# Optimization experiments

Measured on AMD Instinct MI355X. Metric: run time of the kernel, lower is better.

## Reference

```python
import jax, jax.numpy as jnp
import numpy as np
from jax import lax

DG = 16          # deformable_groups
K = 9            # 3x3 kernel taps
PAD = 1
MAX_RES = 10.0   # max_residue_magnitude


def conv3x3(x, w, b):
    # NCHW / OIHW, stride 1, SAME padding (pad=1 for 3x3)
    return lax.conv_general_dilated(x, w, (1, 1), 'SAME',
                                    dimension_numbers=('NCHW', 'OIHW', 'NCHW')) + b[None, :, None, None]


def lrelu(x):
    return jnp.where(x >= 0, x, 0.1 * x)


def setup_inputs() -> dict:
    key = jax.random.key(0)
    ks = jax.random.split(key, 10)
    B, C, H, W = 4, 64, 128, 128
    Cout = 64
    coff_in = 2 * C + 2          # (1 + pa_frames//2)*C + pa_frames, pa_frames=2
    nch = 3 * K * DG             # 432 offset/mask channels

    def mkw(k, o, i, scale=1.0):
        return jax.random.normal(k, (o, i, 3, 3), jnp.float32) * (scale / np.sqrt(i * 9))

    return {
        'x': jax.random.normal(ks[0], (B, C, H, W), jnp.float32),
        'x_flow_warped': jax.random.normal(ks[1], (B, C, H, W), jnp.float32),
        'x_current': jax.random.normal(ks[2], (B, C, H, W), jnp.float32),
        'flow': jax.random.normal(ks[3], (B, 2, H, W), jnp.float32) * 2.0,
        'w1': mkw(ks[4], Cout, coff_in), 'b1': jnp.zeros((Cout,), jnp.float32),
        'w2': mkw(ks[5], Cout, Cout),    'b2': jnp.zeros((Cout,), jnp.float32),
        'w3': mkw(ks[6], Cout, Cout),    'b3': jnp.zeros((Cout,), jnp.float32),
        'w4': mkw(ks[7], nch, Cout, 0.1), 'b4': jnp.zeros((nch,), jnp.float32),
        'weight': mkw(ks[8], Cout, C),   'bias': jnp.zeros((Cout,), jnp.float32),
    }


def deform_conv2d(x, offset, mask, weight, bias):
    # modulated deformable conv, 3x3, stride 1, pad 1, dilation 1, groups=1
    B, C, H, W = x.shape
    O = weight.shape[0]
    dg, Cg = DG, C // DG
    off = offset.reshape(B, dg, K, 2, H, W)
    dy, dx = off[:, :, :, 0], off[:, :, :, 1]        # (B,dg,K,H,W), (y,x) pairs
    ki = jnp.arange(3)
    ii, jj = jnp.meshgrid(ki, ki, indexing='ij')
    ii = ii.reshape(K).astype(jnp.float32)
    jj = jj.reshape(K).astype(jnp.float32)
    # sampling coords in input space: h - pad + i + dy, w - pad + j + dx
    py = dy + (jnp.arange(H, dtype=jnp.float32) - PAD)[None, None, None, :, None] + ii[None, None, :, None, None]
    px = dx + (jnp.arange(W, dtype=jnp.float32) - PAD)[None, None, None, None, :] + jj[None, None, :, None, None]
    y0 = jnp.floor(py)
    x0 = jnp.floor(px)
    wy1 = py - y0
    wx1 = px - x0
    y0i = y0.astype(jnp.int32)
    x0i = x0.astype(jnp.int32)
    xg = x.reshape(B, dg, Cg, H * W)

    def gather(yi, xi):
        valid = ((yi >= 0) & (yi < H) & (xi >= 0) & (xi < W)).astype(x.dtype)  # zero outside
        idx = (jnp.clip(yi, 0, H - 1) * W + jnp.clip(xi, 0, W - 1)).reshape(B, dg, 1, K * H * W)
        v = jnp.take_along_axis(xg, jnp.broadcast_to(idx, (B, dg, Cg, K * H * W)), axis=-1)
        return v.reshape(B, dg, Cg, K, H, W) * valid[:, :, None]

    s = (gather(y0i, x0i)         * ((1 - wy1) * (1 - wx1))[:, :, None]
         + gather(y0i, x0i + 1)   * ((1 - wy1) * wx1)[:, :, None]
         + gather(y0i + 1, x0i)   * (wy1 * (1 - wx1))[:, :, None]
         + gather(y0i + 1, x0i + 1) * (wy1 * wx1)[:, :, None])
    s = s * mask.reshape(B, dg, 1, K, H, W)
    s = s.reshape(B, C, K, H, W)
    return jnp.einsum('bckhw,ock->bohw', s, weight.reshape(O, C, K)) + bias[None, :, None, None]


def reference(x, x_flow_warped, x_current, flow, w1, b1, w2, b2, w3, b3, w4, b4, weight, bias):
    feat = jnp.concatenate([x_flow_warped, x_current, flow], axis=1)
    h = lrelu(conv3x3(feat, w1, b1))
    h = lrelu(conv3x3(h, w2, b2))
    h = lrelu(conv3x3(h, w3, b3))
    out = conv3x3(h, w4, b4)
    o1, o2, mask = jnp.split(out, 3, axis=1)
    offset = MAX_RES * jnp.tanh(jnp.concatenate([o1, o2], axis=1))
    flowf = flow[:, ::-1]  # flip (x,y) -> (y,x)
    offset = offset + jnp.tile(flowf, (1, offset.shape[1] // 2, 1, 1))
    mask = jax.nn.sigmoid(mask)
    return deform_conv2d(x, offset, mask, weight, bias)
```

## Files before the change

### kernel.cpp

```cpp
#include <hip/hip_runtime.h>
#include <math.h>
#include <type_traits>

#define BH 4
#define HH 128
#define WW 128
#define HW (HH * WW)
#define SSTR 600

typedef __attribute__((ext_vector_type(8))) short bf16x8;
typedef __attribute__((ext_vector_type(4))) float f32x4;

typedef const __attribute__((address_space(1))) void* as1_t;
typedef __attribute__((address_space(3))) void* as3_t;

__device__ inline short f2bf(float f) {
    union { float f; unsigned u; } x; x.f = f;
    unsigned r = x.u + 0x7fff + ((x.u >> 16) & 1);
    return (short)(r >> 16);
}
__device__ inline float bf2f(short h) {
    union { unsigned u; float f; } x; x.u = ((unsigned)(unsigned short)h) << 16;
    return x.f;
}
__device__ inline float bflo(unsigned u) {
    union { unsigned u; float f; } x; x.u = u << 16; return x.f;
}
__device__ inline float bfhi(unsigned u) {
    union { unsigned u; float f; } x; x.u = u & 0xffff0000u; return x.f;
}

struct RepackArgs {
    const float* w[5];
    short* dst[5];
    short* zero;
    int off[6];
};

__device__ inline void repack_generic(const float* w, short* dst, int g,
                                      int M, int Cin, int T, int MT)
{
    int lane = g & 63;
    int f = g >> 6;
    int mt = f % MT;
    int kt = f / MT;
    int tap = kt % T;
    int kc = kt / T;
    int m = mt * 16 + (lane & 15);
    int ic0 = kc * 32 + (lane >> 4) * 8;
    short v[8];
#pragma unroll
    for (int i = 0; i < 8; ++i) {
        int ic = ic0 + i;
        float x = (m < M && ic < Cin) ? w[((size_t)m * Cin + ic) * T + tap] : 0.f;
        v[i] = f2bf(x);
    }
    *(bf16x8*)(dst + (size_t)g * 8) = *(const bf16x8*)v;
}

__global__ __launch_bounds__(256) void repack_all_k(RepackArgs a)
{
    int g = blockIdx.x * 256 + threadIdx.x;
    if (g < a.off[1]) {
        repack_generic(a.w[0], a.dst[0], g - a.off[0], 64, 130, 9, 4);
    } else if (g < a.off[2]) {
        repack_generic(a.w[1], a.dst[1], g - a.off[1], 64, 64, 9, 4);
    } else if (g < a.off[3]) {
        repack_generic(a.w[2], a.dst[2], g - a.off[2], 64, 64, 9, 4);
    } else if (g < a.off[4]) {
        repack_generic(a.w[3], a.dst[3], g - a.off[3], 432, 64, 9, 27);
    } else if (g < a.off[5]) {
        int gg = g - a.off[4];
        int lane = gg & 63;
        int f = gg >> 6;
        int mt = f & 3, kc = f >> 2;
        int m = mt * 16 + (lane & 15);
        int ck0 = kc * 32 + (lane >> 4) * 8;
        short v[8];
#pragma unroll
        for (int i = 0; i < 8; ++i) {
            int ck = ck0 + i;
            int dg = ck / 36, rem = ck % 36;
            int k = rem >> 2, cg = rem & 3;
            int c = dg * 4 + cg;
            v[i] = f2bf(a.w[4][((size_t)m * 64 + c) * 9 + k]);
        }
        *(bf16x8*)(a.dst[4] + (size_t)gg * 8) = *(const bf16x8*)v;
    } else if (g < a.off[5] + 8) {
        uint2 z; z.x = 0; z.y = 0;
        *(uint2*)(a.zero + (size_t)(g - a.off[5]) * 4) = z;
    }
}

__global__ __launch_bounds__(256) void prep_k(
    const float* __restrict__ xfw, const float* __restrict__ xcur,
    const float* __restrict__ flow, const float* __restrict__ x,
    short* __restrict__ cc, short* __restrict__ xt)
{
    int tid = threadIdx.x;
    int z = blockIdx.z;
    int px = blockIdx.x * 256 + tid;
    if (z < BH) {
        int b = z;
        const float* s0 = xfw + (size_t)b * 64 * HW + px;
        const float* s1 = xcur + (size_t)b * 64 * HW + px;
        const float* s2 = flow + (size_t)b * 2 * HW + px;
        short v[144];
#pragma unroll
        for (int c = 0; c < 64; ++c) v[c] = f2bf(s0[(size_t)c * HW]);
#pragma unroll
        for (int c = 0; c < 64; ++c) v[64 + c] = f2bf(s1[(size_t)c * HW]);
        v[128] = f2bf(s2[0]);
        v[129] = f2bf(s2[HW]);
#pragma unroll
        for (int c = 130; c < 144; ++c) v[c] = 0;
        short* dst = cc + ((size_t)b * HW + px) * 144;
#pragma unroll
        for (int q = 0; q < 18; ++q)
            *(bf16x8*)(dst + q * 8) = *(const bf16x8*)&v[q * 8];
    } else {
        int b = z - BH;
        const float* src = x + (size_t)b * 64 * HW + px;
        short v[64];
#pragma unroll
        for (int c = 0; c < 64; ++c) v[c] = f2bf(src[(size_t)c * HW]);
        short* dstb = xt + (size_t)b * 16 * HW * 4 + (size_t)px * 4;
#pragma unroll
        for (int d = 0; d < 16; ++d)
            *(uint2*)(dstb + (size_t)d * HW * 4) = *(const uint2*)&v[d * 4];
    }
}

template<int CSTR, int KC, bool ACT, int MTW>
__global__ __launch_bounds__(256) void conv_mfma_k(
    const short* __restrict__ in, const short* __restrict__ wp,
    const float* __restrict__ bias, const short* __restrict__ zerobuf,
    short* __restrict__ out, int Cout, int MB, int MT)
{
    __shared__ alignas(16) short X[4 * 198 * 8];
    const int tid = threadIdx.x;
    const int lane = tid & 63, wv = tid >> 6;
    const int x0 = blockIdx.x * 64, y = blockIdx.y;
    const int zb = blockIdx.z;
    const int b = zb / MB, mb = zb % MB;

    int mtg[MTW];
#pragma unroll
    for (int mt = 0; mt < MTW; ++mt) {
        int t = (mb * 4 + wv) * MTW + mt;
        mtg[mt] = (t < MT) ? t : MT - 1;
    }

    const int r = tid / 66, c = tid - r * 66;
    const int yy = y + r - 1, xx = x0 + c - 1;
    const bool stg = (tid < 198);
    const bool inb = stg && (yy >= 0 && yy < HH && xx >= 0 && xx < WW);
    const short* srcp = inb ? (in + ((size_t)b * HW + (size_t)yy * WW + xx) * CSTR)
                            : zerobuf;

    f32x4 acc[MTW][4] = {};

    for (int kc = 0; kc < KC; ++kc) {
        __syncthreads();
        if (stg) {
            const short* gp = inb ? (srcp + kc * 32) : srcp;
#pragma unroll
            for (int g = 0; g < 4; ++g) {
                __builtin_amdgcn_global_load_lds(
                    (as1_t)(const void*)(gp + g * 8),
                    (as3_t)(void*)&X[((size_t)g * 198 + wv * 64) * 8],
                    16, 0, 0);
            }
        }
        __syncthreads();
#pragma unroll
        for (int tap = 0; tap < 9; ++tap) {
            const int dy = tap / 3, dx = tap - dy * 3;
            bf16x8 a[MTW];
#pragma unroll
            for (int mt = 0; mt < MTW; ++mt)
                a[mt] = *(const bf16x8*)(wp + (((size_t)(kc * 9 + tap) * MT + mtg[mt]) * 64 + lane) * 8);
#pragma unroll
            for (int nt = 0; nt < 4; ++nt) {
                int cc2 = nt * 16 + (lane & 15) + dx;
                bf16x8 bb = *(const bf16x8*)&X[(((lane >> 4) * 198) + dy * 66 + cc2) * 8];
#pragma unroll
                for (int mt = 0; mt < MTW; ++mt)
                    acc[mt][nt] = __builtin_amdgcn_mfma_f32_16x16x32_bf16(a[mt], bb, acc[mt][nt], 0, 0, 0);
            }
        }
    }

    const int xl = lane & 15, rg = lane >> 4;
#pragma unroll
    for (int mt = 0; mt < MTW; ++mt) {
        int t = (mb * 4 + wv) * MTW + mt;
        int m0 = t * 16;
        if (m0 >= Cout) continue;
#pragma unroll
        for (int nt = 0; nt < 4; ++nt) {
            int xx2 = x0 + nt * 16 + xl;
            short pk[4];
#pragma unroll
            for (int j = 0; j < 4; ++j) {
                int o = m0 + rg * 4 + j;
                float rv = acc[mt][nt][j] + bias[o];
                if (ACT) rv = (rv >= 0.f) ? rv : 0.1f * rv;
                pk[j] = f2bf(rv);
            }
            *(uint2*)(out + ((size_t)b * HW + (size_t)y * WW + xx2) * (size_t)Cout
                      + m0 + rg * 4) = *(const uint2*)pk;
        }
    }
}

__global__ __launch_bounds__(256) void dcn_k(
    const short* __restrict__ xt, const float* __restrict__ flow,
    const short* __restrict__ out4, const short* __restrict__ wtp,
    const float* __restrict__ bias, float* __restrict__ out)
{
    __shared__ alignas(16) short s[16 * SSTR];
    const int tid = threadIdx.x;
    const int b = blockIdx.z, y = blockIdx.y, xb = blockIdx.x * 16;
    const size_t hw = (size_t)HW;
    constexpr float L2E = 1.4426950408889634f;

    const int lane = tid & 63, wv = tid >> 6;
    const int p = tid & 15;
    const int dg = tid >> 4;
    const int xp = xb + p;
    const size_t pix = (size_t)y * WW + xp;
    const short* xg = xt + ((size_t)b * 16 + dg) * hw * 4;
    const short* o4p = out4 + ((size_t)b * hw + pix) * 432;
    const float fl0 = flow[((size_t)b * 2 + 0) * hw + pix];
    const float fl1 = flow[((size_t)b * 2 + 1) * hw + pix];

    const unsigned* pd = (const unsigned*)o4p + 9 * dg;
    const short* pm = o4p + 288 + 9 * dg;
    short* sp = &s[p * SSTR + dg * 36];

#pragma unroll
    for (int it = 0; it < 9; ++it) {
        unsigned dyx = pd[it];
        float omk = bf2f(pm[it]);
        float ody = bflo(dyx), odx = bfhi(dyx);
        float tdy = 1.f - 2.f * __builtin_amdgcn_rcpf(__builtin_amdgcn_exp2f(2.f * L2E * ody) + 1.f);
        float tdx = 1.f - 2.f * __builtin_amdgcn_rcpf(__builtin_amdgcn_exp2f(2.f * L2E * odx) + 1.f);
        float m   = __builtin_amdgcn_rcpf(1.f + __builtin_amdgcn_exp2f(-L2E * omk));

        float py = 10.f * tdy + fl1 + (float)(y  - 1 + it / 3);
        float px = 10.f * tdx + fl0 + (float)(xp - 1 + it % 3);
        float fy = floorf(py), fx = floorf(px);
        int iy0 = (int)fy, ix0 = (int)fx;
        float wy1 = py - fy, wx1 = px - fx;
        float wy0 = 1.f - wy1, wx0 = 1.f - wx1;
        int iy1 = iy0 + 1, ix1 = ix0 + 1;
        bool vy0 = (iy0 >= 0) & (iy0 < HH), vy1 = (iy1 >= 0) & (iy1 < HH);
        bool vx0 = (ix0 >= 0) & (ix0 < WW), vx1 = (ix1 >= 0) & (ix1 < WW);
        float w00 = (vy0 & vx0) ? wy0 * wx0 : 0.f;
        float w01 = (vy0 & vx1) ? wy0 * wx1 : 0.f;
        float w10 = (vy1 & vx0) ? wy1 * wx0 : 0.f;
        float w11 = (vy1 & vx1) ? wy1 * wx1 : 0.f;
        int cy0 = min(max(iy0, 0), HH - 1), cy1 = min(max(iy1, 0), HH - 1);
        int cx0 = min(max(ix0, 0), WW - 1), cx1 = min(max(ix1, 0), WW - 1);
        uint2 d00 = *(const uint2*)(xg + (size_t)(cy0 * WW + cx0) * 4);
        uint2 d01 = *(const uint2*)(xg + (size_t)(cy0 * WW + cx1) * 4);
        uint2 d10 = *(const uint2*)(xg + (size_t)(cy1 * WW + cx0) * 4);
        uint2 d11 = *(const uint2*)(xg + (size_t)(cy1 * WW + cx1) * 4);

        float a0 = w00 * bflo(d00.x) + w01 * bflo(d01.x) + w10 * bflo(d10.x) + w11 * bflo(d11.x);
        float a1 = w00 * bfhi(d00.x) + w01 * bfhi(d01.x) + w10 * bfhi(d10.x) + w11 * bfhi(d11.x);
        float a2 = w00 * bflo(d00.y) + w01 * bflo(d01.y) + w10 * bflo(d10.y) + w11 * bflo(d11.y);
        float a3 = w00 * bfhi(d00.y) + w01 * bfhi(d01.y) + w10 * bfhi(d10.y) + w11 * bfhi(d11.y);

        uint2 t;
        t.x = ((unsigned)(unsigned short)f2bf(a1 * m) << 16) | (unsigned short)f2bf(a0 * m);
        t.y = ((unsigned)(unsigned short)f2bf(a3 * m) << 16) | (unsigned short)f2bf(a2 * m);
        *(uint2*)&sp[it * 4] = t;
    }
    __syncthreads();

    f32x4 acc = {};
#pragma unroll
    for (int kc = 0; kc < 18; ++kc) {
        bf16x8 a = *(const bf16x8*)(wtp + ((size_t)(kc * 4 + wv) * 64 + lane) * 8);
        bf16x8 bb = *(const bf16x8*)&s[(lane & 15) * SSTR + kc * 32 + (lane >> 4) * 8];
        acc = __builtin_amdgcn_mfma_f32_16x16x32_bf16(a, bb, acc, 0, 0, 0);
    }

    const int xl = lane & 15, rg = lane >> 4;
#pragma unroll
    for (int j = 0; j < 4; ++j) {
        int o = wv * 16 + rg * 4 + j;
        out[((size_t)(b * 64 + o) * HH + y) * WW + xb + xl] = acc[j] + bias[o];
    }
}

extern "C" void kernel_launch(void* const* d_in, const int* in_sizes, int n_in,
                              void* d_out, int out_size, void* d_ws, size_t ws_size,
                              hipStream_t stream)
{
    const float* x    = (const float*)d_in[0];
    const float* xfw  = (const float*)d_in[1];
    const float* xcur = (const float*)d_in[2];
    const float* flow = (const float*)d_in[3];
    const float* w1   = (const float*)d_in[4];
    const float* b1   = (const float*)d_in[5];
    const float* w2   = (const float*)d_in[6];
    const float* b2   = (const float*)d_in[7];
    const float* w3   = (const float*)d_in[8];
    const float* b3   = (const float*)d_in[9];
    const float* w4   = (const float*)d_in[10];
    const float* b4   = (const float*)d_in[11];
    const float* wt   = (const float*)d_in[12];
    const float* bs   = (const float*)d_in[13];

    const size_t hw = (size_t)HW;
    short* out4 = (short*)d_ws;
    short* h1   = out4 + (size_t)BH * hw * 432;
    short* h2   = h1 + (size_t)BH * hw * 64;
    short* cc   = h2 + (size_t)BH * hw * 64;
    short* xt   = cc + (size_t)BH * hw * 144 + 256;
    short* wp1  = xt + (size_t)BH * hw * 64 + 256;
    short* wp2  = wp1 + (size_t)180 * 512;
    short* wp3  = wp2 + (size_t)72 * 512;
    short* wp4  = wp3 + (size_t)72 * 512;
    short* wtp  = wp4 + (size_t)486 * 512;
    short* zb   = wtp + (size_t)72 * 512;

    RepackArgs ra;
    ra.w[0] = w1; ra.w[1] = w2; ra.w[2] = w3; ra.w[3] = w4; ra.w[4] = wt;
    ra.dst[0] = wp1; ra.dst[1] = wp2; ra.dst[2] = wp3; ra.dst[3] = wp4; ra.dst[4] = wtp;
    ra.zero = zb;
    int tot[5] = {11520, 4608, 4608, 31104, 4608};
    ra.off[0] = 0;
    for (int i = 0; i < 5; ++i) ra.off[i + 1] = ra.off[i] + tot[i];
    repack_all_k<<<(ra.off[5] + 8 + 255) / 256, 256, 0, stream>>>(ra);

    prep_k<<<dim3(HW / 256, 1, 2 * BH), 256, 0, stream>>>(xfw, xcur, flow, x, cc, xt);

    dim3 blk(256);
    conv_mfma_k<144, 5, true,  1><<<dim3(2, 128, BH),     blk, 0, stream>>>(cc, wp1, b1, zb, h1, 64, 1, 4);
    conv_mfma_k<64,  2, true,  1><<<dim3(2, 128, BH),     blk, 0, stream>>>(h1, wp2, b2, zb, h2, 64, 1, 4);
    conv_mfma_k<64,  2, true,  1><<<dim3(2, 128, BH),     blk, 0, stream>>>(h2, wp3, b3, zb, h1, 64, 1, 4);
    conv_mfma_k<64,  2, false, 4><<<dim3(2, 128, BH * 2), blk, 0, stream>>>(h1, wp4, b4, zb, out4, 432, 2, 27);

    dcn_k<<<dim3(WW / 16, HH, BH), blk, 0, stream>>>(xt, flow, out4, wtp, bs, (float*)d_out);
}
```

Measured before the change: 210.6 us.

## Retile conv kernels so each wave computes four output-channel tiles over a full row

```diff
diff --git a/kernel.cpp b/kernel.cpp
--- a/kernel.cpp
+++ b/kernel.cpp
@@ -86,7 +86,7 @@
             v[i] = f2bf(a.w[4][((size_t)m * 64 + c) * 9 + k]);
         }
         *(bf16x8*)(a.dst[4] + (size_t)gg * 8) = *(const bf16x8*)v;
-    } else if (g < a.off[5] + 8) {
+    } else if (g < a.off[5] + 48) {
         uint2 z; z.x = 0; z.y = 0;
         *(uint2*)(a.zero + (size_t)(g - a.off[5]) * 4) = z;
     }
@@ -131,61 +131,71 @@
     }
 }
 
-template<int CSTR, int KC, bool ACT, int MTW>
-__global__ __launch_bounds__(256) void conv_mfma_k(
+template<int CSTR, int KC, bool ACT>
+__global__ __launch_bounds__(128) void conv_mfma_k(
     const short* __restrict__ in, const short* __restrict__ wp,
     const float* __restrict__ bias, const short* __restrict__ zerobuf,
-    short* __restrict__ out, int Cout, int MB, int MT)
-{
-    __shared__ alignas(16) short X[4 * 198 * 8];
+    short* __restrict__ out, int Cout, int MG, int MT)
+{
+    __shared__ alignas(16) short X[4 * 390 * 8];
     const int tid = threadIdx.x;
     const int lane = tid & 63, wv = tid >> 6;
-    const int x0 = blockIdx.x * 64, y = blockIdx.y;
+    const int y = blockIdx.y;
     const int zb = blockIdx.z;
-    const int b = zb / MB, mb = zb % MB;
-
-    int mtg[MTW];
-#pragma unroll
-    for (int mt = 0; mt < MTW; ++mt) {
-        int t = (mb * 4 + wv) * MTW + mt;
+    const int b = zb / MG, mg = zb % MG;
+
+    int mtg[4];
+#pragma unroll
+    for (int mt = 0; mt < 4; ++mt) {
+        int t = mg * 4 + mt;
         mtg[mt] = (t < MT) ? t : MT - 1;
     }
 
-    const int r = tid / 66, c = tid - r * 66;
-    const int yy = y + r - 1, xx = x0 + c - 1;
-    const bool stg = (tid < 198);
-    const bool inb = stg && (yy >= 0 && yy < HH && xx >= 0 && xx < WW);
-    const short* srcp = inb ? (in + ((size_t)b * HW + (size_t)yy * WW + xx) * CSTR)
-                            : zerobuf;
-
-    f32x4 acc[MTW][4] = {};
+    const short* sp_[4];
+    bool act_[4];
+#pragma unroll
+    for (int it = 0; it < 4; ++it) {
+        int px = it * 128 + tid;
+        int r = px / 130, c = px - r * 130;
+        int yy = y + r - 1, xx = c - 1;
+        bool act = (px < 390);
+        bool inb = act && (yy >= 0 && yy < HH && xx >= 0 && xx < WW);
+        sp_[it] = inb ? (in + ((size_t)b * HW + (size_t)yy * WW + xx) * CSTR)
+                      : zerobuf;
+        act_[it] = act;
+    }
+
+    f32x4 acc[4][4] = {};
 
     for (int kc = 0; kc < KC; ++kc) {
         __syncthreads();
-        if (stg) {
-            const short* gp = inb ? (srcp + kc * 32) : srcp;
-#pragma unroll
-            for (int g = 0; g < 4; ++g) {
-                __builtin_amdgcn_global_load_lds(
-                    (as1_t)(const void*)(gp + g * 8),
-                    (as3_t)(void*)&X[((size_t)g * 198 + wv * 64) * 8],
-                    16, 0, 0);
+#pragma unroll
+        for (int it = 0; it < 4; ++it) {
+            if (act_[it]) {
+                const short* gp = sp_[it] + kc * 32;
+#pragma unroll
+                for (int g = 0; g < 4; ++g) {
+                    __builtin_amdgcn_global_load_lds(
+                        (as1_t)(const void*)(gp + g * 8),
+                        (as3_t)(void*)&X[((size_t)g * 390 + it * 128 + wv * 64) * 8],
+                        16, 0, 0);
+                }
             }
         }
         __syncthreads();
 #pragma unroll
         for (int tap = 0; tap < 9; ++tap) {
             const int dy = tap / 3, dx = tap - dy * 3;
-            bf16x8 a[MTW];
-#pragma unroll
-            for (int mt = 0; mt < MTW; ++mt)
+            bf16x8 a[4];
+#pragma unroll
+            for (int mt = 0; mt < 4; ++mt)
                 a[mt] = *(const bf16x8*)(wp + (((size_t)(kc * 9 + tap) * MT + mtg[mt]) * 64 + lane) * 8);
 #pragma unroll
             for (int nt = 0; nt < 4; ++nt) {
-                int cc2 = nt * 16 + (lane & 15) + dx;
-                bf16x8 bb = *(const bf16x8*)&X[(((lane >> 4) * 198) + dy * 66 + cc2) * 8];
-#pragma unroll
-                for (int mt = 0; mt < MTW; ++mt)
+                int col = wv * 64 + nt * 16 + (lane & 15) + dx;
+                bf16x8 bb = *(const bf16x8*)&X[(((lane >> 4) * 390) + dy * 130 + col) * 8];
+#pragma unroll
+                for (int mt = 0; mt < 4; ++mt)
                     acc[mt][nt] = __builtin_amdgcn_mfma_f32_16x16x32_bf16(a[mt], bb, acc[mt][nt], 0, 0, 0);
             }
         }
@@ -193,13 +203,14 @@
 
     const int xl = lane & 15, rg = lane >> 4;
 #pragma unroll
-    for (int mt = 0; mt < MTW; ++mt) {
-        int t = (mb * 4 + wv) * MTW + mt;
+    for (int mt = 0; mt < 4; ++mt) {
+        int t = mg * 4 + mt;
+        if (t >= MT) continue;
         int m0 = t * 16;
         if (m0 >= Cout) continue;
 #pragma unroll
         for (int nt = 0; nt < 4; ++nt) {
-            int xx2 = x0 + nt * 16 + xl;
+            int xx2 = wv * 64 + nt * 16 + xl;
             short pk[4];
 #pragma unroll
             for (int j = 0; j < 4; ++j) {
@@ -335,15 +346,14 @@
     int tot[5] = {11520, 4608, 4608, 31104, 4608};
     ra.off[0] = 0;
     for (int i = 0; i < 5; ++i) ra.off[i + 1] = ra.off[i] + tot[i];
-    repack_all_k<<<(ra.off[5] + 8 + 255) / 256, 256, 0, stream>>>(ra);
+    repack_all_k<<<(ra.off[5] + 48 + 255) / 256, 256, 0, stream>>>(ra);
 
     prep_k<<<dim3(HW / 256, 1, 2 * BH), 256, 0, stream>>>(xfw, xcur, flow, x, cc, xt);
 
-    dim3 blk(256);
-    conv_mfma_k<144, 5, true,  1><<<dim3(2, 128, BH),     blk, 0, stream>>>(cc, wp1, b1, zb, h1, 64, 1, 4);
-    conv_mfma_k<64,  2, true,  1><<<dim3(2, 128, BH),     blk, 0, stream>>>(h1, wp2, b2, zb, h2, 64, 1, 4);
-    conv_mfma_k<64,  2, true,  1><<<dim3(2, 128, BH),     blk, 0, stream>>>(h2, wp3, b3, zb, h1, 64, 1, 4);
-    conv_mfma_k<64,  2, false, 4><<<dim3(2, 128, BH * 2), blk, 0, stream>>>(h1, wp4, b4, zb, out4, 432, 2, 27);
-
-    dcn_k<<<dim3(WW / 16, HH, BH), blk, 0, stream>>>(xt, flow, out4, wtp, bs, (float*)d_out);
-}
+    conv_mfma_k<144, 5, true ><<<dim3(1, 128, BH),     dim3(128), 0, stream>>>(cc, wp1, b1, zb, h1, 64, 1, 4);
+    conv_mfma_k<64,  2, true ><<<dim3(1, 128, BH),     dim3(128), 0, stream>>>(h1, wp2, b2, zb, h2, 64, 1, 4);
+    conv_mfma_k<64,  2, true ><<<dim3(1, 128, BH),     dim3(128), 0, stream>>>(h2, wp3, b3, zb, h1, 64, 1, 4);
+    conv_mfma_k<64,  2, false><<<dim3(1, 128, BH * 7), dim3(128), 0, stream>>>(h1, wp4, b4, zb, out4, 432, 7, 27);
+
+    dcn_k<<<dim3(WW / 16, HH, BH), dim3(256), 0, stream>>>(xt, flow, out4, wtp, bs, (float*)d_out);
+}
```

After: 229.5 us. +9.0%, slower.
